# Performance work log

Hardware: AMD Instinct MI355X
Metric: run time of the kernel (lower is better)

## Reference

```python
import jax, jax.numpy as jnp
import numpy as np

B, N, CQ, H, CH = 1, 256, 128, 4, 32  # batch, n_res, c_q(=c_k=c_v), heads, per-head dim


def setup_inputs() -> dict:
    key = jax.random.key(0)
    ks = jax.random.split(key, 12)
    s = 0.02
    q_x = jax.random.normal(ks[0], (B, N, N, CQ), jnp.float32)
    kv_x = jax.random.normal(ks[1], (B, N, N, CQ), jnp.float32)
    # mask bias: 0 where kept, -1e9 where masked (additive mask)
    keep = jax.random.uniform(ks[2], (B, N, 1, 1, N)) < 0.9
    mask_bias = jnp.where(keep, 0.0, -1e9).astype(jnp.float32)
    triangle_bias = jax.random.normal(ks[3], (B, 1, H, N, N), jnp.float32)
    # projection weights, stored per-head as [H, CH, C_in]
    wq = jax.random.normal(ks[4], (H, CH, CQ), jnp.float32) * s
    wk = jax.random.normal(ks[5], (H, CH, CQ), jnp.float32) * s
    wv = jax.random.normal(ks[6], (H, CH, CQ), jnp.float32) * s
    wg = jax.random.normal(ks[7], (H, CH, CQ), jnp.float32) * s
    bg = jax.random.normal(ks[8], (H, CH), jnp.float32) * s + 1.0  # gating bias init 1
    wo = jax.random.normal(ks[9], (CQ, H * CH), jnp.float32) * s
    bo = jnp.zeros((CQ,), jnp.float32)
    return {"q_x": q_x, "kv_x": kv_x, "mask_bias": mask_bias,
            "triangle_bias": triangle_bias, "wq": wq, "wk": wk, "wv": wv,
            "wg": wg, "bg": bg, "wo": wo, "bo": bo}


def reference(q_x, kv_x, mask_bias, triangle_bias, wq, wk, wv, wg, bg, wo, bo):
    scale = 1.0 / np.sqrt(CH).astype(np.float32)
    # project + split heads: [B,N,Q,C] x [H,D,C] -> [B,N,H,Q,D]
    q = jnp.einsum('bnqc,hdc->bnhqd', q_x, wq) * scale
    k = jnp.einsum('bnkc,hdc->bnhkd', kv_x, wk)
    v = jnp.einsum('bnkc,hdc->bnhkd', kv_x, wv)
    # scores + additive biases (mask_bias broadcasts over h,q; triangle over n)
    a = jnp.einsum('bnhqd,bnhkd->bnhqk', q, k) + mask_bias + triangle_bias
    a = jax.nn.softmax(a, axis=-1)
    o = jnp.einsum('bnhqk,bnhkd->bnhqd', a, v)
    o = jnp.swapaxes(o, -2, -3)  # [B,N,Q,H,D]
    # gating
    g = jax.nn.sigmoid(jnp.einsum('bnqc,hdc->bnqhd', q_x, wg) + bg)
    o = o * g
    o = o.reshape(o.shape[:-2] + (H * CH,))  # [B,N,Q,H*D]
    return jnp.einsum('bnqe,ce->bnqc', o, wo) + bo
```

## Files before the change

kernel.cpp:

```cpp
#include <hip/hip_runtime.h>

#define NRES 256
#define CIN  128
#define NH   4
#define DH   32

typedef __attribute__((ext_vector_type(4))) float f32x4;
typedef __attribute__((ext_vector_type(8))) short bf16x8;
typedef unsigned short u16;

#define U_WQG 0
#define U_WKV 32768
#define U_WWO 65536
#define U_QB  131072
#define U_KB  (U_QB + 8388608)
#define U_VT  (U_KB + 8388608)
#define U_GB  (U_VT + 8388608)
#define WS_NEED ((size_t)(U_GB + 8388608) * 2)

__device__ __forceinline__ unsigned pkbf(float a, float b) {
    unsigned ua = __builtin_bit_cast(unsigned, a);
    unsigned ub = __builtin_bit_cast(unsigned, b);
    ua += 0x7fffu + ((ua >> 16) & 1u);
    ub += 0x7fffu + ((ub >> 16) & 1u);
    return __builtin_amdgcn_perm(ub, ua, 0x07060302);
}
__device__ __forceinline__ u16 f2bfu(float f) {
    unsigned u = __builtin_bit_cast(unsigned, f);
    return (u16)((u + 0x7fffu + ((u >> 16) & 1u)) >> 16);
}
__device__ __forceinline__ float bf2f(u16 v) {
    unsigned u = ((unsigned)v) << 16;
    return __builtin_bit_cast(float, u);
}
union bfr { unsigned u[4]; bf16x8 v; };
__device__ __forceinline__ bf16x8 ldcvt8(const float* __restrict__ p) {
    f32x4 a = *(const f32x4*)p; f32x4 b = *(const f32x4*)(p + 4);
    bfr r;
    r.u[0] = pkbf(a[0], a[1]); r.u[1] = pkbf(a[2], a[3]);
    r.u[2] = pkbf(b[0], b[1]); r.u[3] = pkbf(b[2], b[3]);
    return r.v;
}
__device__ __forceinline__ bf16x8 ldcvt8s(const float* __restrict__ p, float sc) {
    f32x4 a = *(const f32x4*)p; f32x4 b = *(const f32x4*)(p + 4);
    bfr r;
    r.u[0] = pkbf(a[0] * sc, a[1] * sc); r.u[1] = pkbf(a[2] * sc, a[3] * sc);
    r.u[2] = pkbf(b[0] * sc, b[1] * sc); r.u[3] = pkbf(b[2] * sc, b[3] * sc);
    return r.v;
}
#define MFMA(a, b, c) __builtin_amdgcn_mfma_f32_16x16x32_bf16((a), (b), (c), 0, 0, 0)

__global__ void wconv(const float* __restrict__ wq, const float* __restrict__ wk,
                      const float* __restrict__ wv, const float* __restrict__ wg,
                      const float* __restrict__ wo, u16* __restrict__ ws)
{
    const int i0 = (blockIdx.x * 256 + threadIdx.x) * 8;
    const float qsc = 0.17677669529663687f;
    const float* src; u16* dst; float sc = 1.f;
    if (i0 < 32768) {
        const int e = i0 >> 7, c = i0 & 127;
        src = (e < 128 ? wq + e * CIN : wg + (e - 128) * CIN) + c;
        if (e < 128) sc = qsc;
        dst = ws + U_WQG + i0;
    } else if (i0 < 65536) {
        const int j = i0 - 32768, e = j >> 7, c = j & 127;
        src = (e < 128 ? wk + e * CIN : wv + (e - 128) * CIN) + c;
        dst = ws + U_WKV + j;
    } else {
        const int j = i0 - 65536;
        src = wo + j; dst = ws + U_WWO + j;
    }
    *(bf16x8*)dst = ldcvt8s(src, sc);
}

#define AST 136
__global__ __launch_bounds__(256, 3) void proj(
    const float* __restrict__ q_x, const float* __restrict__ kv_x,
    const float* __restrict__ bg, u16* __restrict__ ws)
{
    const int t = threadIdx.x, lane = t & 63, w = t >> 6;
    const int mrow = lane & 15, grp = lane >> 4;
    const int koff = grp * 8, rbase = grp * 4;
    const int R0 = blockIdx.x * 64;
    const int e0 = w * 64;
    const int ysel = blockIdx.y;
    const float* __restrict__ src = ysel ? kv_x : q_x;
    const u16* __restrict__ W = ws + (ysel ? U_WKV : U_WQG);
    const bool vpath = (ysel == 1) && (w >= 2);

    __shared__ u16 As[64 * AST];

    {
        const int srow = w * 16 + mrow;
        const float* __restrict__ sp = src + (size_t)(R0 + srow) * CIN + grp * 32;
        u16* __restrict__ dp = &As[srow * AST + grp * 32];
        #pragma unroll
        for (int cc = 0; cc < 4; ++cc)
            *(bf16x8*)(dp + cc * 8) = ldcvt8(sp + cc * 8);
    }

    const f32x4 zf = {0.f, 0.f, 0.f, 0.f};
    f32x4 acc[4][4];
    #pragma unroll
    for (int mt = 0; mt < 4; ++mt)
        #pragma unroll
        for (int nt = 0; nt < 4; ++nt) acc[mt][nt] = zf;

    bf16x8 bw0 = *(const bf16x8*)(W + (e0 +  0 + mrow) * CIN + koff);
    bf16x8 bw1 = *(const bf16x8*)(W + (e0 + 16 + mrow) * CIN + koff);
    bf16x8 bw2 = *(const bf16x8*)(W + (e0 + 32 + mrow) * CIN + koff);
    bf16x8 bw3 = *(const bf16x8*)(W + (e0 + 48 + mrow) * CIN + koff);

    __syncthreads();

    if (!vpath) {
        #pragma unroll 1
        for (int ct = 0; ct < 4; ++ct) {
            const int c0n = ((ct + 1) & 3) * 32 + koff;
            const bf16x8 nb0 = *(const bf16x8*)(W + (e0 +  0 + mrow) * CIN + c0n);
            const bf16x8 nb1 = *(const bf16x8*)(W + (e0 + 16 + mrow) * CIN + c0n);
            const bf16x8 nb2 = *(const bf16x8*)(W + (e0 + 32 + mrow) * CIN + c0n);
            const bf16x8 nb3 = *(const bf16x8*)(W + (e0 + 48 + mrow) * CIN + c0n);
            const int c0 = ct * 32 + koff;
            #pragma unroll
            for (int mt = 0; mt < 4; ++mt) {
                const bf16x8 aX = *(const bf16x8*)&As[(mt * 16 + mrow) * AST + c0];
                acc[mt][0] = MFMA(bw0, aX, acc[mt][0]);
                acc[mt][1] = MFMA(bw1, aX, acc[mt][1]);
                acc[mt][2] = MFMA(bw2, aX, acc[mt][2]);
                acc[mt][3] = MFMA(bw3, aX, acc[mt][3]);
            }
            bw0 = nb0; bw1 = nb1; bw2 = nb2; bw3 = nb3;
        }
    } else {
        #pragma unroll 1
        for (int ct = 0; ct < 4; ++ct) {
            const int c0n = ((ct + 1) & 3) * 32 + koff;
            const bf16x8 nb0 = *(const bf16x8*)(W + (e0 +  0 + mrow) * CIN + c0n);
            const bf16x8 nb1 = *(const bf16x8*)(W + (e0 + 16 + mrow) * CIN + c0n);
            const bf16x8 nb2 = *(const bf16x8*)(W + (e0 + 32 + mrow) * CIN + c0n);
            const bf16x8 nb3 = *(const bf16x8*)(W + (e0 + 48 + mrow) * CIN + c0n);
            const int c0 = ct * 32 + koff;
            #pragma unroll
            for (int mt = 0; mt < 4; ++mt) {
                const bf16x8 aX = *(const bf16x8*)&As[(mt * 16 + mrow) * AST + c0];
                acc[mt][0] = MFMA(aX, bw0, acc[mt][0]);
                acc[mt][1] = MFMA(aX, bw1, acc[mt][1]);
                acc[mt][2] = MFMA(aX, bw2, acc[mt][2]);
                acc[mt][3] = MFMA(aX, bw3, acc[mt][3]);
            }
            bw0 = nb0; bw1 = nb1; bw2 = nb2; bw3 = nb3;
        }
    }

    if (!ysel) {
        if (w < 2) {
            #pragma unroll
            for (int mt = 0; mt < 4; ++mt) {
                const size_t row = (size_t)(R0 + mt * 16 + mrow);
                #pragma unroll
                for (int nt = 0; nt < 4; ++nt) {
                    uint2 v;
                    v.x = pkbf(acc[mt][nt][0], acc[mt][nt][1]);
                    v.y = pkbf(acc[mt][nt][2], acc[mt][nt][3]);
                    *(uint2*)&ws[U_QB + row * CIN + e0 + nt * 16 + rbase] = v;
                }
            }
        } else {
            #pragma unroll
            for (int mt = 0; mt < 4; ++mt) {
                const size_t row = (size_t)(R0 + mt * 16 + mrow);
                #pragma unroll
                for (int nt = 0; nt < 4; ++nt) {
                    const int eb = (e0 - 128) + nt * 16 + rbase;
                    const f32x4 bgv = *(const f32x4*)(bg + eb);
                    float g[4];
                    #pragma unroll
                    for (int r = 0; r < 4; ++r)
                        g[r] = 1.f / (1.f + __expf(-(acc[mt][nt][r] + bgv[r])));
                    uint2 v;
                    v.x = pkbf(g[0], g[1]);
                    v.y = pkbf(g[2], g[3]);
                    *(uint2*)&ws[U_GB + row * CIN + eb] = v;
                }
            }
        }
    } else {
        if (w < 2) {
            #pragma unroll
            for (int mt = 0; mt < 4; ++mt) {
                const size_t row = (size_t)(R0 + mt * 16 + mrow);
                #pragma unroll
                for (int nt = 0; nt < 4; ++nt) {
                    uint2 v;
                    v.x = pkbf(acc[mt][nt][0], acc[mt][nt][1]);
                    v.y = pkbf(acc[mt][nt][2], acc[mt][nt][3]);
                    *(uint2*)&ws[U_KB + row * CIN + e0 + nt * 16 + rbase] = v;
                }
            }
        } else {
            const int n = R0 >> 8;
            #pragma unroll
            for (int mt = 0; mt < 4; ++mt) {
                const int k0 = (R0 & 255) + mt * 16 + rbase;
                #pragma unroll
                for (int nt = 0; nt < 4; ++nt) {
                    const int d = (e0 - 128) + nt * 16 + mrow;
                    uint2 v;
                    v.x = pkbf(acc[mt][nt][0], acc[mt][nt][1]);
                    v.y = pkbf(acc[mt][nt][2], acc[mt][nt][3]);
                    *(uint2*)&ws[U_VT + ((size_t)n * 128 + d) * 256 + k0] = v;
                }
            }
        }
    }
}

#define PST 40
__global__ __launch_bounds__(128, 4) void flash(
    u16* __restrict__ ws, const float* __restrict__ mask_bias,
    const float* __restrict__ tri_bias)
{
    const int h = blockIdx.x, n = blockIdx.y;
    const int t = threadIdx.x, lane = t & 63, w = t >> 6;
    const int mrow = lane & 15, grp = lane >> 4;
    const int koff = grp * 8, rbase = grp * 4;
    const int q0 = ((int)blockIdx.z * 2 + w) * 64;

    __shared__ u16 Pt[2 * 64 * PST];
    __shared__ float msk[NRES];

    if (t < 64) {
        float4 mv = *(const float4*)(mask_bias + n * NRES + t * 4);
        mv.x -= 8.f; mv.y -= 8.f; mv.z -= 8.f; mv.w -= 8.f;
        *(float4*)&msk[t * 4] = mv;
    }

    u16* __restrict__ QOg = ws + U_QB + (size_t)n * NRES * CIN;
    const u16* __restrict__ Kb = ws + U_KB + (size_t)n * NRES * CIN;
    const u16* __restrict__ Vt = ws + U_VT + (size_t)n * 128 * 256;
    const u16* __restrict__ Gb = ws + U_GB + (size_t)n * NRES * CIN;
    const float* __restrict__ trih = tri_bias + (size_t)h * NRES * NRES;

    bf16x8 aq[4];
    #pragma unroll
    for (int qt = 0; qt < 4; ++qt)
        aq[qt] = *(const bf16x8*)(QOg + (size_t)(q0 + qt * 16 + mrow) * CIN + h * DH + koff);

    bf16x8 bk0 = *(const bf16x8*)(Kb + (size_t)(mrow) * CIN + h * DH + koff);
    bf16x8 bk1 = *(const bf16x8*)(Kb + (size_t)(16 + mrow) * CIN + h * DH + koff);
    bf16x8 bv0 = *(const bf16x8*)(Vt + (size_t)(h * DH + mrow) * NRES + koff);
    bf16x8 bv1 = *(const bf16x8*)(Vt + (size_t)(h * DH + 16 + mrow) * NRES + koff);

    __syncthreads();

    const f32x4 zf = {0.f, 0.f, 0.f, 0.f};
    f32x4 oa[4][2];
    float ls[4];
    #pragma unroll
    for (int qt = 0; qt < 4; ++qt) { oa[qt][0] = zf; oa[qt][1] = zf; ls[qt] = 0.f; }

    u16* __restrict__ pw = &Pt[w * 64 * PST];

    #pragma unroll 1
    for (int kt = 0; kt < 8; ++kt) {
        const int kb = kt * 32;
        const f32x4 m0 = *(const f32x4*)&msk[kb + rbase];
        const f32x4 m1 = *(const f32x4*)&msk[kb + 16 + rbase];

        #pragma unroll
        for (int qt = 0; qt < 4; ++qt) {
            const int q = q0 + qt * 16 + mrow;
            const f32x4 t0 = *(const f32x4*)(trih + (size_t)q * NRES + kb + rbase);
            const f32x4 t1 = *(const f32x4*)(trih + (size_t)q * NRES + kb + 16 + rbase);
            f32x4 s0 = MFMA(bk0, aq[qt], zf);
            f32x4 s1 = MFMA(bk1, aq[qt], zf);
            float part = 0.f;
            #pragma unroll
            for (int r = 0; r < 4; ++r) {
                s0[r] = __expf(s0[r] + t0[r] + m0[r]);
                s1[r] = __expf(s1[r] + t1[r] + m1[r]);
                part += s0[r] + s1[r];
            }
            ls[qt] += part;
            uint2 v0, v1;
            v0.x = pkbf(s0[0], s0[1]); v0.y = pkbf(s0[2], s0[3]);
            v1.x = pkbf(s1[0], s1[1]); v1.y = pkbf(s1[2], s1[3]);
            *(uint2*)&pw[(qt * 16 + mrow) * PST + rbase]      = v0;
            *(uint2*)&pw[(qt * 16 + mrow) * PST + 16 + rbase] = v1;
        }

        const int kbn = ((kt + 1) & 7) * 32;
        const bf16x8 nbk0 = *(const bf16x8*)(Kb + (size_t)(kbn + mrow) * CIN + h * DH + koff);
        const bf16x8 nbk1 = *(const bf16x8*)(Kb + (size_t)(kbn + 16 + mrow) * CIN + h * DH + koff);
        const bf16x8 nbv0 = *(const bf16x8*)(Vt + (size_t)(h * DH + mrow) * NRES + kbn + koff);
        const bf16x8 nbv1 = *(const bf16x8*)(Vt + (size_t)(h * DH + 16 + mrow) * NRES + kbn + koff);

        asm volatile("s_waitcnt lgkmcnt(0)" ::: "memory");
        __builtin_amdgcn_sched_barrier(0);
        #pragma unroll
        for (int qt = 0; qt < 4; ++qt) {
            bf16x8 pa = *(const bf16x8*)&pw[(qt * 16 + mrow) * PST + koff];
            oa[qt][0] = MFMA(bv0, pa, oa[qt][0]);
            oa[qt][1] = MFMA(bv1, pa, oa[qt][1]);
        }
        bk0 = nbk0; bk1 = nbk1; bv0 = nbv0; bv1 = nbv1;
    }

    #pragma unroll
    for (int qt = 0; qt < 4; ++qt) {
        float lv = ls[qt];
        lv += __shfl_xor(lv, 16, 64);
        lv += __shfl_xor(lv, 32, 64);
        const float inv = 1.f / lv;
        const int q = q0 + qt * 16 + mrow;
        #pragma unroll
        for (int half = 0; half < 2; ++half) {
            const size_t off = (size_t)q * CIN + h * DH + half * 16 + rbase;
            const uint2 gv = *(const uint2*)&Gb[off];
            const float g0 = bf2f((u16)(gv.x)),        g1 = bf2f((u16)(gv.x >> 16));
            const float g2 = bf2f((u16)(gv.y)),        g3 = bf2f((u16)(gv.y >> 16));
            uint2 ov;
            ov.x = pkbf(oa[qt][half][0] * inv * g0, oa[qt][half][1] * inv * g1);
            ov.y = pkbf(oa[qt][half][2] * inv * g2, oa[qt][half][3] * inv * g3);
            *(uint2*)&QOg[off] = ov;
        }
    }
}

__global__ __launch_bounds__(256, 4) void gout(
    const u16* __restrict__ ws, const float* __restrict__ bo,
    float* __restrict__ out)
{
    const int t = threadIdx.x, lane = t & 63, w = t >> 6;
    const int mrow = lane & 15, grp = lane >> 4;
    const int koff = grp * 8, rbase = grp * 4;
    const int r0 = blockIdx.x * 128 + w * 32;
    const u16* __restrict__ Wo = ws + U_WWO;
    const u16* __restrict__ QOg = ws + U_QB;

    const f32x4 zf = {0.f, 0.f, 0.f, 0.f};
    f32x4 acc[2][8];
    #pragma unroll
    for (int at = 0; at < 2; ++at)
        #pragma unroll
        for (int nt = 0; nt < 8; ++nt) acc[at][nt] = zf;

    #pragma unroll
    for (int ks = 0; ks < 4; ++ks) {
        const int e0 = ks * 32 + koff;
        const bf16x8 a0 = *(const bf16x8*)(QOg + (size_t)(r0 + mrow) * CIN + e0);
        const bf16x8 a1 = *(const bf16x8*)(QOg + (size_t)(r0 + 16 + mrow) * CIN + e0);
        #pragma unroll
        for (int nt = 0; nt < 8; ++nt) {
            const bf16x8 bw = *(const bf16x8*)(Wo + (nt * 16 + mrow) * CIN + e0);
            acc[0][nt] = MFMA(bw, a0, acc[0][nt]);
            acc[1][nt] = MFMA(bw, a1, acc[1][nt]);
        }
    }

    #pragma unroll
    for (int nt = 0; nt < 8; ++nt) {
        const f32x4 bov = *(const f32x4*)&bo[nt * 16 + rbase];
        #pragma unroll
        for (int at = 0; at < 2; ++at) {
            const f32x4 v = acc[at][nt] + bov;
            *(f32x4*)&out[(size_t)(r0 + at * 16 + mrow) * CIN + nt * 16 + rbase] = v;
        }
    }
}

#define KST 32
#define VST 264
#define GST 136

__global__ __launch_bounds__(256, 3) void attn_fb(
    const float* __restrict__ q_x, const float* __restrict__ kv_x,
    const float* __restrict__ mask_bias, const float* __restrict__ tri_bias,
    const float* __restrict__ wq, const float* __restrict__ wk,
    const float* __restrict__ wv, float* __restrict__ o_out)
{
    const int h = blockIdx.x, n = blockIdx.y;
    const int t = threadIdx.x;
    const int lane = t & 63, w = t >> 6;
    const int mrow = lane & 15;
    const int grp  = lane >> 4;
    const int koff = grp * 8;
    const int rbase = grp * 4;
    const int q0 = w * 64;

    __shared__ u16 Ks[NRES * KST];
    __shared__ u16 Vt[DH * VST];
    __shared__ u16 Ptb[4 * 32 * PST];
    __shared__ float msk[NRES];

    if (t < 64) *(float4*)&msk[t * 4] = *(const float4*)(mask_bias + n * NRES + t * 4);

    const float* __restrict__ qxn = q_x  + (size_t)n * NRES * CIN;
    const float* __restrict__ kxn = kv_x + (size_t)n * NRES * CIN;
    const float* __restrict__ wqh = wq + h * DH * CIN;
    const float* __restrict__ wkh = wk + h * DH * CIN;
    const float* __restrict__ wvh = wv + h * DH * CIN;

    f32x4 aq_[4][2], ak_[4][2], av_[4][2];
    const f32x4 zf = {0.f, 0.f, 0.f, 0.f};
    #pragma unroll
    for (int qt = 0; qt < 4; ++qt)
        #pragma unroll
        for (int dt = 0; dt < 2; ++dt) { aq_[qt][dt] = zf; ak_[qt][dt] = zf; av_[qt][dt] = zf; }

    const float qsc = 0.17677669529663687f;
    #pragma unroll
    for (int ct = 0; ct < 4; ++ct) {
        const int c0 = ct * 32 + koff;
        bf16x8 bq0 = ldcvt8s(wqh + mrow * CIN + c0, qsc);
        bf16x8 bq1 = ldcvt8s(wqh + (16 + mrow) * CIN + c0, qsc);
        bf16x8 bk0 = ldcvt8(wkh + mrow * CIN + c0);
        bf16x8 bk1 = ldcvt8(wkh + (16 + mrow) * CIN + c0);
        bf16x8 bv0 = ldcvt8(wvh + mrow * CIN + c0);
        bf16x8 bv1 = ldcvt8(wvh + (16 + mrow) * CIN + c0);
        #pragma unroll
        for (int qt = 0; qt < 4; ++qt) {
            bf16x8 aX = ldcvt8(qxn + (q0 + qt * 16 + mrow) * CIN + c0);
            aq_[qt][0] = MFMA(aX, bq0, aq_[qt][0]);
            aq_[qt][1] = MFMA(aX, bq1, aq_[qt][1]);
            bf16x8 aK = ldcvt8(kxn + (q0 + qt * 16 + mrow) * CIN + c0);
            ak_[qt][0] = MFMA(aK, bk0, ak_[qt][0]);
            ak_[qt][1] = MFMA(aK, bk1, ak_[qt][1]);
            av_[qt][0] = MFMA(aK, bv0, av_[qt][0]);
            av_[qt][1] = MFMA(aK, bv1, av_[qt][1]);
        }
    }

    #pragma unroll
    for (int qt = 0; qt < 4; ++qt)
        #pragma unroll
        for (int dt = 0; dt < 2; ++dt)
            #pragma unroll
            for (int r = 0; r < 4; ++r) {
                const int row = q0 + qt * 16 + rbase + r;
                const int d = dt * 16 + mrow;
                Ks[row * KST + d] = f2bfu(ak_[qt][dt][r]);
                Vt[d * VST + row] = f2bfu(av_[qt][dt][r]);
            }

    u16* __restrict__ pw = &Ptb[w * 32 * PST];
    bf16x8 aq[4];
    #pragma unroll
    for (int h2 = 0; h2 < 2; ++h2) {
        #pragma unroll
        for (int j = 0; j < 2; ++j) {
            const int qt = h2 * 2 + j;
            #pragma unroll
            for (int dt = 0; dt < 2; ++dt)
                #pragma unroll
                for (int r = 0; r < 4; ++r)
                    pw[(j * 16 + rbase + r) * PST + dt * 16 + mrow] = f2bfu(aq_[qt][dt][r]);
        }
        asm volatile("s_waitcnt lgkmcnt(0)" ::: "memory");
        #pragma unroll
        for (int j = 0; j < 2; ++j)
            aq[h2 * 2 + j] = *(const bf16x8*)&pw[(j * 16 + mrow) * PST + koff];
        asm volatile("s_waitcnt lgkmcnt(0)" ::: "memory");
    }
    __syncthreads();

    f32x4 oa[4][2], ls4[4];
    #pragma unroll
    for (int qt = 0; qt < 4; ++qt) { oa[qt][0] = zf; oa[qt][1] = zf; ls4[qt] = zf; }

    const float* __restrict__ trih = tri_bias + (size_t)h * NRES * NRES;

    for (int kt = 0; kt < 8; ++kt) {
        const int kb = kt * 32;
        bf16x8 bk0 = *(const bf16x8*)&Ks[(kb + mrow) * KST + koff];
        bf16x8 bk1 = *(const bf16x8*)&Ks[(kb + 16 + mrow) * KST + koff];
        bf16x8 bv0 = *(const bf16x8*)&Vt[mrow * VST + kb + koff];
        bf16x8 bv1 = *(const bf16x8*)&Vt[(16 + mrow) * VST + kb + koff];
        const float mb0 = msk[kb + mrow] - 8.f;
        const float mb1 = msk[kb + 16 + mrow] - 8.f;

        #pragma unroll
        for (int h2 = 0; h2 < 2; ++h2) {
            float tr0[2][4], tr1[2][4];
            #pragma unroll
            for (int j = 0; j < 2; ++j) {
                const int qt = h2 * 2 + j;
                const float* __restrict__ trow =
                    trih + (q0 + qt * 16 + rbase) * NRES + kb + mrow;
                #pragma unroll
                for (int r = 0; r < 4; ++r) {
                    tr0[j][r] = trow[r * NRES];
                    tr1[j][r] = trow[r * NRES + 16];
                }
            }
            #pragma unroll
            for (int j = 0; j < 2; ++j) {
                const int qt = h2 * 2 + j;
                f32x4 s0 = MFMA(aq[qt], bk0, zf);
                f32x4 s1 = MFMA(aq[qt], bk1, zf);
                #pragma unroll
                for (int r = 0; r < 4; ++r) {
                    s0[r] = __expf(s0[r] + tr0[j][r] + mb0);
                    s1[r] = __expf(s1[r] + tr1[j][r] + mb1);
                }
                ls4[qt] += s0 + s1;
                #pragma unroll
                for (int r = 0; r < 4; ++r) {
                    pw[(j * 16 + rbase + r) * PST + mrow]      = f2bfu(s0[r]);
                    pw[(j * 16 + rbase + r) * PST + 16 + mrow] = f2bfu(s1[r]);
                }
            }
            asm volatile("s_waitcnt lgkmcnt(0)" ::: "memory");
            #pragma unroll
            for (int j = 0; j < 2; ++j) {
                const int qt = h2 * 2 + j;
                bf16x8 pa = *(const bf16x8*)&pw[(j * 16 + mrow) * PST + koff];
                oa[qt][0] = MFMA(pa, bv0, oa[qt][0]);
                oa[qt][1] = MFMA(pa, bv1, oa[qt][1]);
            }
        }
    }

    float* __restrict__ orow = o_out + (size_t)n * NRES * CIN + h * DH;
    #pragma unroll
    for (int qt = 0; qt < 4; ++qt) {
        f32x4 lv = ls4[qt];
        #pragma unroll
        for (int xm = 1; xm < 16; xm <<= 1) {
            lv[0] += __shfl_xor(lv[0], xm, 64);
            lv[1] += __shfl_xor(lv[1], xm, 64);
            lv[2] += __shfl_xor(lv[2], xm, 64);
            lv[3] += __shfl_xor(lv[3], xm, 64);
        }
        #pragma unroll
        for (int r = 0; r < 4; ++r) {
            const float inv = 1.f / lv[r];
            const int q = q0 + qt * 16 + rbase + r;
            orow[q * CIN + mrow]      = oa[qt][0][r] * inv;
            orow[q * CIN + 16 + mrow] = oa[qt][1][r] * inv;
        }
    }
}

__global__ __launch_bounds__(256, 4) void gate_fb(
    const float* __restrict__ q_x, const float* __restrict__ wg,
    const float* __restrict__ bg, const float* __restrict__ wo,
    const float* __restrict__ bo, float* io)
{
    const int t = threadIdx.x;
    const int lane = t & 63, w = t >> 6;
    const int mrow = lane & 15, grp = lane >> 4;
    const int koff = grp * 8, rbase = grp * 4;
    const int r0 = blockIdx.x * 128 + w * 32;

    __shared__ u16 Gt[4 * 32 * GST];
    u16* __restrict__ gw = &Gt[w * 32 * GST];

    const f32x4 zf = {0.f, 0.f, 0.f, 0.f};
    f32x4 acc[2][8];
    #pragma unroll
    for (int at = 0; at < 2; ++at)
        #pragma unroll
        for (int nt = 0; nt < 8; ++nt) acc[at][nt] = zf;

    #pragma unroll
    for (int ks = 0; ks < 4; ++ks) {
        const int c0 = ks * 32 + koff;
        bf16x8 ax0 = ldcvt8(q_x + (size_t)(r0 + mrow) * CIN + c0);
        bf16x8 ax1 = ldcvt8(q_x + (size_t)(r0 + 16 + mrow) * CIN + c0);
        #pragma unroll
        for (int nt = 0; nt < 8; ++nt) {
            bf16x8 bw = ldcvt8(wg + (nt * 16 + mrow) * CIN + c0);
            acc[0][nt] = MFMA(ax0, bw, acc[0][nt]);
            acc[1][nt] = MFMA(ax1, bw, acc[1][nt]);
        }
    }

    #pragma unroll
    for (int nt = 0; nt < 8; ++nt) {
        const float bge = bg[nt * 16 + mrow];
        #pragma unroll
        for (int at = 0; at < 2; ++at)
            #pragma unroll
            for (int r = 0; r < 4; ++r) {
                const int qg = r0 + at * 16 + rbase + r;
                const float ov = io[(size_t)qg * CIN + nt * 16 + mrow];
                const float g = 1.f / (1.f + __expf(-(acc[at][nt][r] + bge)));
                gw[(at * 16 + rbase + r) * GST + nt * 16 + mrow] = f2bfu(ov * g);
            }
    }
    asm volatile("s_waitcnt lgkmcnt(0)" ::: "memory");

    f32x4 acc2[2][8];
    #pragma unroll
    for (int at = 0; at < 2; ++at)
        #pragma unroll
        for (int nt = 0; nt < 8; ++nt) acc2[at][nt] = zf;

    #pragma unroll
    for (int ks = 0; ks < 4; ++ks) {
        const int e0 = ks * 32 + koff;
        bf16x8 ag0 = *(const bf16x8*)&gw[mrow * GST + e0];
        bf16x8 ag1 = *(const bf16x8*)&gw[(16 + mrow) * GST + e0];
        #pragma unroll
        for (int nt = 0; nt < 8; ++nt) {
            bf16x8 bw = ldcvt8(wo + (nt * 16 + mrow) * CIN + e0);
            acc2[0][nt] = MFMA(ag0, bw, acc2[0][nt]);
            acc2[1][nt] = MFMA(ag1, bw, acc2[1][nt]);
        }
    }

    #pragma unroll
    for (int nt = 0; nt < 8; ++nt) {
        const float boc = bo[nt * 16 + mrow];
        #pragma unroll
        for (int at = 0; at < 2; ++at)
            #pragma unroll
            for (int r = 0; r < 4; ++r)
                io[(size_t)(r0 + at * 16 + rbase + r) * CIN + nt * 16 + mrow] =
                    acc2[at][nt][r] + boc;
    }
}

extern "C" void kernel_launch(void* const* d_in, const int* in_sizes, int n_in,
                              void* d_out, int out_size, void* d_ws, size_t ws_size,
                              hipStream_t stream) {
    const float* q_x  = (const float*)d_in[0];
    const float* kv_x = (const float*)d_in[1];
    const float* mask = (const float*)d_in[2];
    const float* tri  = (const float*)d_in[3];
    const float* wq   = (const float*)d_in[4];
    const float* wk   = (const float*)d_in[5];
    const float* wv   = (const float*)d_in[6];
    const float* wg   = (const float*)d_in[7];
    const float* bg   = (const float*)d_in[8];
    const float* wo   = (const float*)d_in[9];
    const float* bo   = (const float*)d_in[10];
    float* out = (float*)d_out;

    if (ws_size >= WS_NEED) {
        u16* ws16 = (u16*)d_ws;
        wconv<<<40, 256, 0, stream>>>(wq, wk, wv, wg, wo, ws16);
        proj<<<dim3(1024, 2), 256, 0, stream>>>(q_x, kv_x, bg, ws16);
        flash<<<dim3(NH, NRES, 2), 128, 0, stream>>>(ws16, mask, tri);
        gout<<<512, 256, 0, stream>>>(ws16, bo, out);
    } else {
        attn_fb<<<dim3(NH, NRES), 256, 0, stream>>>(q_x, kv_x, mask, tri, wq, wk, wv, out);
        gate_fb<<<(NRES * NRES) / 128, 256, 0, stream>>>(q_x, wg, bg, wo, bo, out);
    }
}
```

Measured before the change: 228.0 us.

## Feed softmax probabilities to PV MFMA from registers, dropping the LDS round-trip

The flash kernel no longer writes the exponentiated scores to shared memory and reads them back transposed. It uses the QK^T MFMA output layout directly as the A operand of 16x16x16 bf16 MFMAs, splitting each 32-key step into two K=16 halves with matching V loads. This removes the LDS stores, the lgkmcnt wait and the sched barrier. In exchange it issues twice as many smaller MFMAs for PV and drops the software prefetch of the next K/V tiles, which are now loaded at the top of each iteration.

```diff
diff --git a/kernel.cpp b/kernel.cpp
--- a/kernel.cpp
+++ b/kernel.cpp
@@ -7,6 +7,7 @@
 
 typedef __attribute__((ext_vector_type(4))) float f32x4;
 typedef __attribute__((ext_vector_type(8))) short bf16x8;
+typedef __attribute__((ext_vector_type(4))) short bf16x4;
 typedef unsigned short u16;
 
 #define U_WQG 0
@@ -49,6 +50,17 @@
     return r.v;
 }
 #define MFMA(a, b, c) __builtin_amdgcn_mfma_f32_16x16x32_bf16((a), (b), (c), 0, 0, 0)
+
+__device__ __forceinline__ f32x4 MFMA16(bf16x4 a, bf16x4 b, f32x4 c) {
+#if __has_builtin(__builtin_amdgcn_mfma_f32_16x16x16bf16_1k)
+    return __builtin_amdgcn_mfma_f32_16x16x16bf16_1k(a, b, c, 0, 0, 0);
+#else
+    f32x4 d;
+    asm volatile("v_mfma_f32_16x16x16_bf16 %0, %1, %2, %3"
+                 : "=v"(d) : "v"(a), "v"(b), "v"(c));
+    return d;
+#endif
+}
 
 __global__ void wconv(const float* __restrict__ wq, const float* __restrict__ wk,
                       const float* __restrict__ wv, const float* __restrict__ wg,
@@ -216,7 +228,6 @@
     }
 }
 
-#define PST 40
 __global__ __launch_bounds__(128, 4) void flash(
     u16* __restrict__ ws, const float* __restrict__ mask_bias,
     const float* __restrict__ tri_bias)
@@ -227,7 +238,6 @@
     const int koff = grp * 8, rbase = grp * 4;
     const int q0 = ((int)blockIdx.z * 2 + w) * 64;
 
-    __shared__ u16 Pt[2 * 64 * PST];
     __shared__ float msk[NRES];
 
     if (t < 64) {
@@ -247,11 +257,6 @@
     for (int qt = 0; qt < 4; ++qt)
         aq[qt] = *(const bf16x8*)(QOg + (size_t)(q0 + qt * 16 + mrow) * CIN + h * DH + koff);
 
-    bf16x8 bk0 = *(const bf16x8*)(Kb + (size_t)(mrow) * CIN + h * DH + koff);
-    bf16x8 bk1 = *(const bf16x8*)(Kb + (size_t)(16 + mrow) * CIN + h * DH + koff);
-    bf16x8 bv0 = *(const bf16x8*)(Vt + (size_t)(h * DH + mrow) * NRES + koff);
-    bf16x8 bv1 = *(const bf16x8*)(Vt + (size_t)(h * DH + 16 + mrow) * NRES + koff);
-
     __syncthreads();
 
     const f32x4 zf = {0.f, 0.f, 0.f, 0.f};
@@ -260,11 +265,15 @@
     #pragma unroll
     for (int qt = 0; qt < 4; ++qt) { oa[qt][0] = zf; oa[qt][1] = zf; ls[qt] = 0.f; }
 
-    u16* __restrict__ pw = &Pt[w * 64 * PST];
-
     #pragma unroll 1
     for (int kt = 0; kt < 8; ++kt) {
         const int kb = kt * 32;
+        bf16x8 bk0 = *(const bf16x8*)(Kb + (size_t)(kb + mrow) * CIN + h * DH + koff);
+        bf16x8 bk1 = *(const bf16x8*)(Kb + (size_t)(kb + 16 + mrow) * CIN + h * DH + koff);
+        const bf16x4 bvL0 = *(const bf16x4*)(Vt + (size_t)(h * DH + mrow) * NRES + kb + rbase);
+        const bf16x4 bvH0 = *(const bf16x4*)(Vt + (size_t)(h * DH + mrow) * NRES + kb + 16 + rbase);
+        const bf16x4 bvL1 = *(const bf16x4*)(Vt + (size_t)(h * DH + 16 + mrow) * NRES + kb + rbase);
+        const bf16x4 bvH1 = *(const bf16x4*)(Vt + (size_t)(h * DH + 16 + mrow) * NRES + kb + 16 + rbase);
         const f32x4 m0 = *(const f32x4*)&msk[kb + rbase];
         const f32x4 m1 = *(const f32x4*)&msk[kb + 16 + rbase];
 
@@ -283,28 +292,14 @@
                 part += s0[r] + s1[r];
             }
             ls[qt] += part;
-            uint2 v0, v1;
-            v0.x = pkbf(s0[0], s0[1]); v0.y = pkbf(s0[2], s0[3]);
-            v1.x = pkbf(s1[0], s1[1]); v1.y = pkbf(s1[2], s1[3]);
-            *(uint2*)&pw[(qt * 16 + mrow) * PST + rbase]      = v0;
-            *(uint2*)&pw[(qt * 16 + mrow) * PST + 16 + rbase] = v1;
-        }
-
-        const int kbn = ((kt + 1) & 7) * 32;
-        const bf16x8 nbk0 = *(const bf16x8*)(Kb + (size_t)(kbn + mrow) * CIN + h * DH + koff);
-        const bf16x8 nbk1 = *(const bf16x8*)(Kb + (size_t)(kbn + 16 + mrow) * CIN + h * DH + koff);
-        const bf16x8 nbv0 = *(const bf16x8*)(Vt + (size_t)(h * DH + mrow) * NRES + kbn + koff);
-        const bf16x8 nbv1 = *(const bf16x8*)(Vt + (size_t)(h * DH + 16 + mrow) * NRES + kbn + koff);
-
-        asm volatile("s_waitcnt lgkmcnt(0)" ::: "memory");
-        __builtin_amdgcn_sched_barrier(0);
-        #pragma unroll
-        for (int qt = 0; qt < 4; ++qt) {
-            bf16x8 pa = *(const bf16x8*)&pw[(qt * 16 + mrow) * PST + koff];
-            oa[qt][0] = MFMA(bv0, pa, oa[qt][0]);
-            oa[qt][1] = MFMA(bv1, pa, oa[qt][1]);
-        }
-        bk0 = nbk0; bk1 = nbk1; bv0 = nbv0; bv1 = nbv1;
+            union { unsigned u[2]; bf16x4 v; } p0, p1;
+            p0.u[0] = pkbf(s0[0], s0[1]); p0.u[1] = pkbf(s0[2], s0[3]);
+            p1.u[0] = pkbf(s1[0], s1[1]); p1.u[1] = pkbf(s1[2], s1[3]);
+            oa[qt][0] = MFMA16(bvL0, p0.v, oa[qt][0]);
+            oa[qt][0] = MFMA16(bvH0, p1.v, oa[qt][0]);
+            oa[qt][1] = MFMA16(bvL1, p0.v, oa[qt][1]);
+            oa[qt][1] = MFMA16(bvH1, p1.v, oa[qt][1]);
+        }
     }
 
     #pragma unroll
@@ -370,6 +365,7 @@
     }
 }
 
+#define PST 40
 #define KST 32
 #define VST 264
 #define GST 136
```

Result: slower. 235.1 us (+3.1%).
